# Kernel optimization log

Measured on AMD Instinct MI355X. Metric: run time of the kernel, lower is better.

## Reference

```python
import jax, jax.numpy as jnp
import numpy as np

EMBED = 512
HEADS = 8
HEAD_DIM = EMBED // HEADS
SCALE_BASE = 512
NEG = -1e9


def xpos_apply(x, offset, downscale):
    # x: [(b h), L, d]
    L, d = x.shape[1], x.shape[2]
    min_pos = -(L + offset) // 2
    max_pos = L + offset + min_pos
    base = (jnp.arange(0, d, 2, dtype=jnp.float32) + 0.4 * d) / (1.4 * d)      # [d/2]
    power = jnp.arange(min_pos, max_pos, dtype=jnp.float32) / SCALE_BASE        # [L']
    scale = base[None, :] ** power[:, None]                                     # [L', d/2]
    half = d // 2
    inv_freq = 1.0 / (10000.0 ** (jnp.arange(half, dtype=jnp.float32) / half))
    sinusoid = jnp.arange(scale.shape[0], dtype=jnp.float32)[:, None] * inv_freq[None, :]
    sin, cos = jnp.sin(sinusoid), jnp.cos(sinusoid)
    # keep last L rows (no-op when offset == 0)
    scale, sin, cos = scale[-L:], sin[-L:], cos[-L:]
    if downscale:
        scale = 1.0 / scale
    sin2 = jnp.repeat(sin * scale, 2, axis=-1)   # duplicate_interleave -> [L, d]
    cos2 = jnp.repeat(cos * scale, 2, axis=-1)
    x1, x2 = x[..., ::2], x[..., 1::2]
    rot = jnp.stack([-x2, x1], axis=-1).reshape(x.shape)  # rotate_every_two
    return x * cos2[None] + rot * sin2[None]


def split_heads(x, b, L):
    # 'b l (h d) -> (b h) l d'
    return x.reshape(b, L, HEADS, HEAD_DIM).transpose(0, 2, 1, 3).reshape(b * HEADS, L, HEAD_DIM)


def setup_inputs() -> dict:
    key = jax.random.key(0)
    ks = jax.random.split(key, 12)
    b, L = 4, 2048
    inp = {
        'query': jax.random.normal(ks[0], (b, L, EMBED), jnp.float32),
        'key': jax.random.normal(ks[1], (b, L, EMBED), jnp.float32),
        'value': jax.random.normal(ks[2], (b, L, EMBED), jnp.float32),
        'key_padding_mask': jnp.zeros((b, L), jnp.bool_),
        'attn_mask': jnp.where(jnp.tril(jnp.ones((L, L), jnp.bool_)), 0.0, NEG).astype(jnp.float32),
    }
    s = 1.0 / np.sqrt(EMBED)
    inp['Wq'] = jax.random.normal(ks[3], (EMBED, EMBED), jnp.float32) * s
    inp['bq'] = jnp.zeros((EMBED,), jnp.float32)
    inp['Wk'] = jax.random.normal(ks[4], (EMBED, EMBED), jnp.float32) * s
    inp['bk'] = jnp.zeros((EMBED,), jnp.float32)
    inp['Wv'] = jax.random.normal(ks[5], (EMBED, EMBED), jnp.float32) * s
    inp['bv'] = jnp.zeros((EMBED,), jnp.float32)
    inp['Wo'] = jax.random.normal(ks[6], (EMBED, EMBED), jnp.float32) * s
    inp['bo'] = jnp.zeros((EMBED,), jnp.float32)
    return inp


def reference(query, key, value, key_padding_mask, attn_mask, Wq, bq, Wk, bk, Wv, bv, Wo, bo):
    b, L, _ = query.shape
    q = split_heads(query @ Wq.T + bq, b, L)
    k = split_heads(key @ Wk.T + bk, b, L)
    v = split_heads(value @ Wv.T + bv, b, L)
    k = xpos_apply(k, 0, True)
    q = xpos_apply(q, 0, False)
    q = q * (HEAD_DIM ** -0.5)
    aw = jnp.einsum('btd,bsd->bts', q, k)                 # [(b h), t, s]
    aw = jnp.nan_to_num(aw) + attn_mask[None]
    aw = aw.reshape(b, HEADS, L, L)
    aw = jnp.where(key_padding_mask[:, None, None, :], jnp.finfo(aw.dtype).min, aw)
    aw = aw.reshape(b * HEADS, L, L)
    probs = jax.nn.softmax(aw.astype(jnp.float32), axis=-1).astype(aw.dtype)
    attn = jnp.einsum('bts,bsd->btd', probs, v)           # [(b h), t, d]
    attn = attn.reshape(b, HEADS, L, HEAD_DIM).transpose(0, 2, 1, 3).reshape(b, L, EMBED)
    return attn @ Wo.T + bo
```

## Files before the change

kernel.cpp:

```cpp
#include <hip/hip_runtime.h>
#include <hip/hip_bf16.h>

typedef __bf16 bf16x2 __attribute__((ext_vector_type(2)));
typedef __bf16 bf16x4 __attribute__((ext_vector_type(4)));
typedef __bf16 bf16x8 __attribute__((ext_vector_type(8)));
typedef float  f32x4  __attribute__((ext_vector_type(4)));

#define SEQ    2048
#define EMB    512
#define NHEAD  8
#define HD     64
#define NBATCH 4
#define MROWS  (NBATCH*SEQ)
#define QSCALE 0.18033688011112042f
#define INV2PI 0.15915494309189535f
#define TWOPI  6.28318530717958648f
#define NEGFREQ (-0.41524101186092028f)

__device__ __forceinline__ f32x4 mfma16(bf16x8 a, bf16x8 b, f32x4 c) {
  return __builtin_amdgcn_mfma_f32_16x16x32_bf16(a, b, c, 0, 0, 0);
}

typedef __attribute__((address_space(1))) const void gv_t;
typedef __attribute__((address_space(3))) void lv_t;
__device__ __forceinline__ void async16(const void* g, void* l) {
  __builtin_amdgcn_global_load_lds((gv_t*)g, (lv_t*)l, 16, 0, 0);
}

__global__ __launch_bounds__(256) void conv_kernel(const float* __restrict__ q,
                                                   const float* __restrict__ k,
                                                   const float* __restrict__ v,
                                                   const float* __restrict__ wq,
                                                   const float* __restrict__ wk,
                                                   const float* __restrict__ wv,
                                                   const float* __restrict__ wo,
                                                   __bf16* __restrict__ Qf,
                                                   __bf16* __restrict__ Kf,
                                                   __bf16* __restrict__ Vf,
                                                   __bf16* __restrict__ Wb,
                                                   float2* __restrict__ qtab,
                                                   float2* __restrict__ ktab) {
  const int z = blockIdx.y;
  if (z == 4) {
    if (blockIdx.x >= 256) return;
    const int t = threadIdx.x;
    const int l = blockIdx.x * 8 + (t >> 5);
    const int i = t & 31;
    const float lf = (float)l;
    const float pw = (lf - 1024.0f) * (1.0f / 512.0f);
    const float lb = __log2f((2.0f * i + 25.6f) * (1.0f / 89.6f));
    const float sc_q = __builtin_amdgcn_exp2f(pw * lb) * QSCALE;
    const float sc_k = __builtin_amdgcn_exp2f(-pw * lb);
    const float ang = lf * __builtin_amdgcn_exp2f((float)i * NEGFREQ);
    float rev = ang * INV2PI;
    rev -= floorf(rev);
    const float ar = rev * TWOPI;
    const float sn = __sinf(ar);
    const float cs = __cosf(ar);
    qtab[l * 32 + i] = float2{ cs * sc_q, sn * sc_q };
    ktab[l * 32 + i] = float2{ cs * sc_k, sn * sc_k };
    return;
  }
  const float* src;
  __bf16* dst;
  size_t i8;
  if (z < 3) {
    src = (z == 0) ? q : (z == 1) ? k : v;
    dst = (z == 0) ? Qf : (z == 1) ? Kf : Vf;
    i8 = ((size_t)blockIdx.x * 256 + threadIdx.x) * 8;
  } else {
    if (blockIdx.x >= 512) return;
    const int zw = blockIdx.x >> 7;
    src = (zw == 0) ? wq : (zw == 1) ? wk : (zw == 2) ? wv : wo;
    dst = Wb + (size_t)zw * (EMB * EMB);
    i8 = ((size_t)(blockIdx.x & 127) * 256 + threadIdx.x) * 8;
  }
  const float4 fa = ((const float4*)(src + i8))[0];
  const float4 fb = ((const float4*)(src + i8))[1];
  bf16x8 h = { (__bf16)fa.x, (__bf16)fa.y, (__bf16)fa.z, (__bf16)fa.w,
               (__bf16)fb.x, (__bf16)fb.y, (__bf16)fb.z, (__bf16)fb.w };
  *(bf16x8*)(dst + i8) = h;
}

__device__ __forceinline__ void gemm_main(const __bf16* __restrict__ A,
                                          const __bf16* __restrict__ W,
                                          __bf16* As, __bf16* Bs,
                                          f32x4 (&acc)[4][4], int m0, int n0) {
  const int tid = threadIdx.x;
  const int wid = tid >> 6, lane = tid & 63;
  const int quad = lane >> 4, l16 = lane & 15;
  const int l7 = l16 & 7;
  const int srow = lane >> 3;
  const int sxor = ((lane & 7) ^ srow) * 8;
  const int wm = (wid >> 1) * 64, wn = (wid & 1) * 64;

  #pragma unroll
  for (int i = 0; i < 4; ++i)
    #pragma unroll
    for (int j = 0; j < 4; ++j) acc[i][j] = (f32x4)(0.0f);

  for (int k0 = 0; k0 < 512; k0 += 64) {
    __syncthreads();
    #pragma unroll
    for (int ii = 0; ii < 4; ++ii) {
      const int r8 = wid * 32 + ii * 8;
      async16(A + (size_t)(m0 + r8 + srow) * 512 + k0 + sxor, &As[r8 * 64]);
      async16(W + (size_t)(n0 + r8 + srow) * 512 + k0 + sxor, &Bs[r8 * 64]);
    }
    __syncthreads();
    #pragma unroll
    for (int ks = 0; ks < 2; ++ks) {
      bf16x8 af[4], bfr[4];
      #pragma unroll
      for (int i = 0; i < 4; ++i)
        af[i] = *(const bf16x8*)&As[(wm + i * 16 + l16) * 64 +
                                    (((quad + ks * 4) ^ l7) * 8)];
      #pragma unroll
      for (int j = 0; j < 4; ++j)
        bfr[j] = *(const bf16x8*)&Bs[(wn + j * 16 + l16) * 64 +
                                     (((quad + ks * 4) ^ l7) * 8)];
      #pragma unroll
      for (int i = 0; i < 4; ++i)
        #pragma unroll
        for (int j = 0; j < 4; ++j)
          acc[i][j] = mfma16(af[i], bfr[j], acc[i][j]);
    }
  }
}

__device__ __forceinline__ void xcd_tile(int& m0, int& n0) {
  const int s = blockIdx.y * 4 + blockIdx.x;
  const int t = s >> 3;
  n0 = (t & 3) * 128;
  m0 = ((s & 7) + ((t >> 2) << 3)) * 128;
}

__global__ __launch_bounds__(256) void gemm_proj_kernel(
    const __bf16* __restrict__ Qf, const __bf16* __restrict__ Kf, const __bf16* __restrict__ Vf,
    const __bf16* __restrict__ Wb,
    const float* __restrict__ bq, const float* __restrict__ bk, const float* __restrict__ bv,
    const float2* __restrict__ qtab, const float2* __restrict__ ktab,
    __bf16* __restrict__ Qx, __bf16* __restrict__ Kx, __bf16* __restrict__ Vt) {
  __shared__ __align__(16) char smem[34816];
  __bf16* As = (__bf16*)smem;
  __bf16* Bs = (__bf16*)(smem + 16384);
  __bf16* T  = (__bf16*)smem;

  const int z = blockIdx.z;
  const __bf16* A = (z == 0) ? Qf : (z == 1) ? Kf : Vf;
  const __bf16* W = Wb + (size_t)z * (EMB * EMB);
  const float* bias = (z == 0) ? bq : (z == 1) ? bk : bv;
  int m0, n0;
  xcd_tile(m0, n0);

  f32x4 acc[4][4];
  gemm_main(A, W, As, Bs, acc, m0, n0);

  const int tid = threadIdx.x;
  const int wid = tid >> 6, lane = tid & 63;
  const int quad = lane >> 4, l16 = lane & 15;
  const int wm = (wid >> 1) * 64, wn = (wid & 1) * 64;

  __syncthreads();

  if (z == 2) {
    #pragma unroll
    for (int j = 0; j < 4; ++j) {
      const float bval = bias[n0 + wn + j * 16 + l16];
      #pragma unroll
      for (int i = 0; i < 4; ++i) {
        bf16x4 p = { (__bf16)(acc[i][j][0] + bval), (__bf16)(acc[i][j][1] + bval),
                     (__bf16)(acc[i][j][2] + bval), (__bf16)(acc[i][j][3] + bval) };
        *(bf16x4*)&T[(wn + j * 16 + l16) * 136 + wm + i * 16 + quad * 4] = p;
      }
    }
    __syncthreads();
    const int nrow = tid >> 1, mh = (tid & 1) << 6;
    bf16x8 vv[8];
    #pragma unroll
    for (int u = 0; u < 8; ++u) vv[u] = *(const bf16x8*)&T[nrow * 136 + mh + u * 8];
    const int n = n0 + nrow, h = n >> 6, d = n & 63;
    const int bb = m0 >> 11, lb2 = (m0 & 2047) + mh;
    __bf16* dst = Vt + ((size_t)(bb * 8 + h) * 64 + d) * 2048 + lb2;
    #pragma unroll
    for (int u = 0; u < 8; ++u) *(bf16x8*)(dst + u * 8) = vv[u];
  } else {
    #pragma unroll
    for (int j = 0; j < 4; ++j) {
      const float bval = bias[n0 + wn + j * 16 + l16];
      #pragma unroll
      for (int i = 0; i < 4; ++i)
        #pragma unroll
        for (int r = 0; r < 4; ++r)
          T[(wm + i * 16 + quad * 4 + r) * 136 + wn + j * 16 + l16] =
              (__bf16)(acc[i][j][r] + bval);
    }
    __syncthreads();
    const int lrow = tid >> 1, half = tid & 1;
    const int gm = m0 + lrow, l = gm & 2047, bb = gm >> 11;
    const int h = (n0 >> 6) + half;
    bf16x8 vv[8];
    #pragma unroll
    for (int u = 0; u < 8; ++u)
      vv[u] = *(const bf16x8*)&T[lrow * 136 + half * 64 + u * 8];
    bf16x8 ov[8];
    const float4* trow = (const float4*)(((z == 0) ? qtab : ktab) + l * 32);
    #pragma unroll
    for (int p = 0; p < 16; ++p) {
      const float4 cs2 = trow[p];
      const int i0 = 2 * p;
      {
        const float x1 = (float)vv[i0 >> 2][(2 * i0) & 7];
        const float x2 = (float)vv[i0 >> 2][(2 * i0 + 1) & 7];
        ov[i0 >> 2][(2 * i0) & 7]     = (__bf16)(x1 * cs2.x - x2 * cs2.y);
        ov[i0 >> 2][(2 * i0 + 1) & 7] = (__bf16)(x2 * cs2.x + x1 * cs2.y);
      }
      {
        const int i1 = i0 + 1;
        const float x1 = (float)vv[i1 >> 2][(2 * i1) & 7];
        const float x2 = (float)vv[i1 >> 2][(2 * i1 + 1) & 7];
        ov[i1 >> 2][(2 * i1) & 7]     = (__bf16)(x1 * cs2.z - x2 * cs2.w);
        ov[i1 >> 2][(2 * i1 + 1) & 7] = (__bf16)(x2 * cs2.z + x1 * cs2.w);
      }
    }
    __bf16* dst = ((z == 0) ? Qx : Kx) + ((size_t)(bb * 8 + h) * 2048 + l) * 64;
    #pragma unroll
    for (int u = 0; u < 8; ++u) *(bf16x8*)(dst + u * 8) = ov[u];
  }
}

__global__ __launch_bounds__(256) void gemm_out_kernel(
    const __bf16* __restrict__ A, const __bf16* __restrict__ W,
    const float* __restrict__ bias, float* __restrict__ C) {
  __shared__ __align__(16) char smem[34816];
  __bf16* As = (__bf16*)smem;
  __bf16* Bs = (__bf16*)(smem + 16384);
  int m0, n0;
  xcd_tile(m0, n0);
  f32x4 acc[4][4];
  gemm_main(A, W, As, Bs, acc, m0, n0);
  const int tid = threadIdx.x;
  const int wid = tid >> 6, lane = tid & 63;
  const int quad = lane >> 4, l16 = lane & 15;
  const int wm = (wid >> 1) * 64, wn = (wid & 1) * 64;
  #pragma unroll
  for (int j = 0; j < 4; ++j) {
    const int n = n0 + wn + j * 16 + l16;
    const float bval = bias[n];
    #pragma unroll
    for (int i = 0; i < 4; ++i)
      #pragma unroll
      for (int r = 0; r < 4; ++r)
        C[(size_t)(m0 + wm + i * 16 + quad * 4 + r) * 512 + n] = acc[i][j][r] + bval;
  }
}

__global__ __launch_bounds__(256) void flash_kernel(const __bf16* __restrict__ Qx,
                                                    const __bf16* __restrict__ Kx,
                                                    const __bf16* __restrict__ Vt,
                                                    const unsigned char* __restrict__ kpm,
                                                    __bf16* __restrict__ Oa) {
  __shared__ __align__(16) __bf16 Ks[2][64 * HD];
  __shared__ __align__(16) __bf16 Vs[2][64 * HD];
  __shared__ __align__(16) __bf16 Qs[64 * HD];

  const int tid = threadIdx.x;
  const int wid = tid >> 6;
  const int lane = tid & 63;
  const int quad = lane >> 4;
  const int l16 = lane & 15;
  const int l7 = l16 & 7;
  const int srow = lane >> 3;
  const int sxor = ((lane & 7) ^ srow) * 8;
  const int bh = blockIdx.x;
  const int b = bh >> 3;
  const int qb = 31 - (int)blockIdx.y;
  const int q0 = qb * 64;

  const __bf16* Qbase = Qx + (size_t)bh * (SEQ * HD);
  const __bf16* Kbase = Kx + (size_t)bh * (SEQ * HD);
  const __bf16* Vbase = Vt + (size_t)bh * (HD * SEQ);
  __bf16* Pw = Qs + wid * 1024;

  #pragma unroll
  for (int ii = 0; ii < 2; ++ii) {
    const int r0 = wid * 16 + ii * 8;
    async16(Qbase + (size_t)(q0 + r0 + srow) * HD + sxor, &Qs[r0 * HD]);
    async16(Kbase + (size_t)(r0 + srow) * HD + sxor, &Ks[0][r0 * HD]);
    async16(Vbase + (size_t)(r0 + srow) * SEQ + sxor, &Vs[0][r0 * HD]);
  }
  __syncthreads();

  const int base0 = (quad ^ l7) * 8;
  const int base1 = ((quad + 4) ^ l7) * 8;
  const int kvo0 = l16 * 64 + base0;
  const int kvo1 = l16 * 64 + base1;

  const bf16x8 qf0 = *(const bf16x8*)&Qs[(wid * 16 + l16) * HD + base0];
  const bf16x8 qf1 = *(const bf16x8*)&Qs[(wid * 16 + l16) * HD + base1];

  __bf16* const pw0 = Pw + l16 * 64 + (((0 + (quad >> 1)) ^ l7) << 3) + (quad & 1) * 4;
  __bf16* const pw1 = Pw + l16 * 64 + (((2 + (quad >> 1)) ^ l7) << 3) + (quad & 1) * 4;
  __bf16* const pw2 = Pw + l16 * 64 + (((4 + (quad >> 1)) ^ l7) << 3) + (quad & 1) * 4;
  __bf16* const pw3 = Pw + l16 * 64 + (((6 + (quad >> 1)) ^ l7) << 3) + (quad & 1) * 4;
  const __bf16* const pr0 = Pw + kvo0;
  const __bf16* const pr1 = Pw + kvo1;

  f32x4 o[4];
  #pragma unroll
  for (int i = 0; i < 4; ++i) o[i] = (f32x4)(0.0f);
  const f32x4 z4 = (f32x4)(0.0f);
  float m_run = -1e30f, l_run = 0.0f;
  const int myq = q0 + wid * 16 + l16;
  const int niter = qb + 1;

  const __bf16* kp0 = Kbase + (size_t)(64 + wid * 16 + srow) * HD + sxor;
  const __bf16* kp1 = kp0 + 8 * HD;
  const __bf16* vp0 = Vbase + (size_t)(wid * 16 + srow) * SEQ + 64 + sxor;
  const __bf16* vp1 = vp0 + 8 * SEQ;
  const unsigned char* kpmb = kpm + b * SEQ + (l16 << 2);

  int it = 0;

#define FLASH_STEP(CUR)                                                        \
  {                                                                            \
    const int kv0 = it << 6;                                                   \
    if (it + 1 < niter) {                                                      \
      async16(kp0, &Ks[1 - (CUR)][(wid * 16 + 0) * HD]);                       \
      async16(kp1, &Ks[1 - (CUR)][(wid * 16 + 8) * HD]);                       \
      async16(vp0, &Vs[1 - (CUR)][(wid * 16 + 0) * HD]);                       \
      async16(vp1, &Vs[1 - (CUR)][(wid * 16 + 8) * HD]);                       \
      kp0 += 64 * HD; kp1 += 64 * HD; vp0 += 64; vp1 += 64;                    \
    }                                                                          \
    const unsigned mine = *(const unsigned*)kpmb;                              \
    f32x4 s[4];                                                                \
    __builtin_amdgcn_s_setprio(1);                                             \
    s[0] = mfma16(*(const bf16x8*)&Ks[CUR][kvo0 +    0], qf0, z4);             \
    s[1] = mfma16(*(const bf16x8*)&Ks[CUR][kvo0 + 1024], qf0, z4);             \
    s[2] = mfma16(*(const bf16x8*)&Ks[CUR][kvo0 + 2048], qf0, z4);             \
    s[3] = mfma16(*(const bf16x8*)&Ks[CUR][kvo0 + 3072], qf0, z4);             \
    s[0] = mfma16(*(const bf16x8*)&Ks[CUR][kvo1 +    0], qf1, s[0]);           \
    s[1] = mfma16(*(const bf16x8*)&Ks[CUR][kvo1 + 1024], qf1, s[1]);           \
    s[2] = mfma16(*(const bf16x8*)&Ks[CUR][kvo1 + 2048], qf1, s[2]);           \
    s[3] = mfma16(*(const bf16x8*)&Ks[CUR][kvo1 + 3072], qf1, s[3]);           \
    __builtin_amdgcn_s_setprio(0);                                             \
                    \
    if (kv0 + 63 > q0 + wid * 16) {                                            \
      _Pragma("unroll")                                                        \
      for (int nb = 0; nb < 4; ++nb)                                           \
        _Pragma("unroll")                                                      \
        for (int r = 0; r < 4; ++r)                                            \
          if (kv0 + nb * 16 + quad * 4 + r > myq) s[nb][r] = -1e30f;           \
    }                                                                          \
                   \
    if (__any(mine != 0)) {                                                    \
      const unsigned char* kq = kpm + b * SEQ + kv0;                           \
      _Pragma("unroll")                                                        \
      for (int nb = 0; nb < 4; ++nb) {                                         \
        const unsigned pk = *(const unsigned*)(kq + nb * 16 + quad * 4);       \
        if (pk) {                                                              \
          if (pk & 0x000000FFu) s[nb][0] = -1e30f;                             \
          if (pk & 0x0000FF00u) s[nb][1] = -1e30f;                             \
          if (pk & 0x00FF0000u) s[nb][2] = -1e30f;                             \
          if (pk & 0xFF000000u) s[nb][3] = -1e30f;                             \
        }                                                                      \
      }                                                                        \
    }                                                                          \
                      \
    float mx;                                                                  \
    {                                                                          \
      f32x4 u0, u1;                                                            \
      _Pragma("unroll")                                                        \
      for (int r = 0; r < 4; ++r) u0[r] = fmaxf(s[0][r], s[1][r]);             \
      _Pragma("unroll")                                                        \
      for (int r = 0; r < 4; ++r) u1[r] = fmaxf(s[2][r], s[3][r]);             \
      _Pragma("unroll")                                                        \
      for (int r = 0; r < 4; ++r) u0[r] = fmaxf(u0[r], u1[r]);                 \
      mx = fmaxf(fmaxf(u0[0], u0[1]), fmaxf(u0[2], u0[3]));                    \
    }                                                                          \
    if (__any(mx > m_run)) {                                                   \
      float rm = fmaxf(mx, __shfl_xor(mx, 16));                                \
      rm = fmaxf(rm, __shfl_xor(rm, 32));                                      \
      const float m_new = fmaxf(m_run, rm);                                    \
      const float alpha = __builtin_amdgcn_exp2f(m_run - m_new);               \
      o[0] *= alpha; o[1] *= alpha; o[2] *= alpha; o[3] *= alpha;              \
      l_run *= alpha;                                                          \
      m_run = m_new;                                                           \
    }                                                                          \
    _Pragma("unroll")                                                          \
    for (int nb = 0; nb < 4; ++nb)                                             \
      _Pragma("unroll")                                                        \
      for (int r = 0; r < 4; ++r)                                              \
        s[nb][r] = __builtin_amdgcn_exp2f(s[nb][r] - m_run);                   \
    {                                                                          \
      f32x4 v01 = s[0] + s[1];                                                 \
      f32x4 v23 = s[2] + s[3];                                                 \
      f32x4 vt = v01 + v23;                                                    \
      l_run += (vt[0] + vt[1]) + (vt[2] + vt[3]);                              \
    }                                                                          \
           \
    *(bf16x4*)pw0 = bf16x4{ (__bf16)s[0][0], (__bf16)s[0][1],                  \
                            (__bf16)s[0][2], (__bf16)s[0][3] };                \
    *(bf16x4*)pw1 = bf16x4{ (__bf16)s[1][0], (__bf16)s[1][1],                  \
                            (__bf16)s[1][2], (__bf16)s[1][3] };                \
    *(bf16x4*)pw2 = bf16x4{ (__bf16)s[2][0], (__bf16)s[2][1],                  \
                            (__bf16)s[2][2], (__bf16)s[2][3] };                \
    *(bf16x4*)pw3 = bf16x4{ (__bf16)s[3][0], (__bf16)s[3][1],                  \
                            (__bf16)s[3][2], (__bf16)s[3][3] };                \
                                     \
    {                                                                          \
      const bf16x8 pf0 = *(const bf16x8*)pr0;                                  \
      __builtin_amdgcn_s_setprio(1);                                           \
      o[0] = mfma16(*(const bf16x8*)&Vs[CUR][kvo0 +    0], pf0, o[0]);         \
      o[1] = mfma16(*(const bf16x8*)&Vs[CUR][kvo0 + 1024], pf0, o[1]);         \
      o[2] = mfma16(*(const bf16x8*)&Vs[CUR][kvo0 + 2048], pf0, o[2]);         \
      o[3] = mfma16(*(const bf16x8*)&Vs[CUR][kvo0 + 3072], pf0, o[3]);         \
      __builtin_amdgcn_s_setprio(0);                                           \
      const bf16x8 pf1 = *(const bf16x8*)pr1;                                  \
      __builtin_amdgcn_s_setprio(1);                                           \
      o[0] = mfma16(*(const bf16x8*)&Vs[CUR][kvo1 +    0], pf1, o[0]);         \
      o[1] = mfma16(*(const bf16x8*)&Vs[CUR][kvo1 + 1024], pf1, o[1]);         \
      o[2] = mfma16(*(const bf16x8*)&Vs[CUR][kvo1 + 2048], pf1, o[2]);         \
      o[3] = mfma16(*(const bf16x8*)&Vs[CUR][kvo1 + 3072], pf1, o[3]);         \
      __builtin_amdgcn_s_setprio(0);                                           \
    }                                                                          \
    kpmb += 64;                                                                \
      \
    if (it + 1 < niter) __syncthreads();                                       \
  }

  while (it + 1 < niter) {
    FLASH_STEP(0);
    ++it;
    FLASH_STEP(1);
    ++it;
  }
  if (it < niter) {
    FLASH_STEP(0);
  }
#undef FLASH_STEP

  float lt = l_run + __shfl_xor(l_run, 16);
  lt += __shfl_xor(lt, 32);

  const float inv_l = 1.0f / lt;
  {
    bf16x4 t0 = { (__bf16)(o[0][0] * inv_l), (__bf16)(o[0][1] * inv_l),
                  (__bf16)(o[0][2] * inv_l), (__bf16)(o[0][3] * inv_l) };
    bf16x4 t1 = { (__bf16)(o[1][0] * inv_l), (__bf16)(o[1][1] * inv_l),
                  (__bf16)(o[1][2] * inv_l), (__bf16)(o[1][3] * inv_l) };
    bf16x4 t2 = { (__bf16)(o[2][0] * inv_l), (__bf16)(o[2][1] * inv_l),
                  (__bf16)(o[2][2] * inv_l), (__bf16)(o[2][3] * inv_l) };
    bf16x4 t3 = { (__bf16)(o[3][0] * inv_l), (__bf16)(o[3][1] * inv_l),
                  (__bf16)(o[3][2] * inv_l), (__bf16)(o[3][3] * inv_l) };
    *(bf16x4*)pw0 = t0;
    *(bf16x4*)pw1 = t1;
    *(bf16x4*)pw2 = t2;
    *(bf16x4*)pw3 = t3;
  }
  const int h = bh & 7;
  #pragma unroll
  for (int ii = 0; ii < 2; ++ii) {
    const int qr = ii * 8 + (lane >> 3);
    const bf16x8 ovv = *(const bf16x8*)&Pw[qr * 64 + (((lane & 7) ^ (qr & 7)) << 3)];
    *(bf16x8*)(Oa + (((size_t)b * SEQ + q0 + wid * 16 + qr) * NHEAD + h) * HD +
               (lane & 7) * 8) = ovv;
  }
}

extern "C" void kernel_launch(void* const* d_in, const int* in_sizes, int n_in,
                              void* d_out, int out_size, void* d_ws, size_t ws_size,
                              hipStream_t stream) {
  (void)in_sizes; (void)n_in; (void)out_size; (void)ws_size;
  const float* query = (const float*)d_in[0];
  const float* key   = (const float*)d_in[1];
  const float* value = (const float*)d_in[2];
  const unsigned char* kpm = (const unsigned char*)d_in[3];
  const float* Wq = (const float*)d_in[5];
  const float* bq = (const float*)d_in[6];
  const float* Wk = (const float*)d_in[7];
  const float* bk = (const float*)d_in[8];
  const float* Wv = (const float*)d_in[9];
  const float* bv = (const float*)d_in[10];
  const float* Wo = (const float*)d_in[11];
  const float* bo = (const float*)d_in[12];
  float* out = (float*)d_out;

  char* ws = (char*)d_ws;
  const size_t SZ = (size_t)MROWS * EMB * 2;
  __bf16* Qf = (__bf16*)(ws);
  __bf16* Kf = (__bf16*)(ws + SZ);
  __bf16* Vf = (__bf16*)(ws + 2 * SZ);
  __bf16* Qx = (__bf16*)(ws + 3 * SZ);
  __bf16* Kx = (__bf16*)(ws + 4 * SZ);
  __bf16* Vt = (__bf16*)(ws + 5 * SZ);
  __bf16* Wb = (__bf16*)(ws + 6 * SZ);
  float2* qtab = (float2*)(ws + 6 * SZ + 4 * (size_t)(EMB * EMB) * 2);
  float2* ktab = qtab + SEQ * 32;
  __bf16* Oa = Qf;

  conv_kernel<<<dim3(2048, 5), dim3(256), 0, stream>>>(
      query, key, value, Wq, Wk, Wv, Wo, Qf, Kf, Vf, Wb, qtab, ktab);
  gemm_proj_kernel<<<dim3(4, 64, 3), dim3(256), 0, stream>>>(
      Qf, Kf, Vf, Wb, bq, bk, bv, qtab, ktab, Qx, Kx, Vt);
  flash_kernel<<<dim3(32, 32), dim3(256), 0, stream>>>(Qx, Kx, Vt, kpm, Oa);
  gemm_out_kernel<<<dim3(4, 64), dim3(256), 0, stream>>>(
      Oa, Wb + (size_t)3 * EMB * EMB, bo, out);
}
```

Measured before the change: 207.5 us.

## Process 128-key tiles per flash iteration with single-buffered synchronous staging

The attention loop now covers 128 keys per iteration instead of 64. It reuses both halves of the K and V shared buffers as one 128-row tile, so there are fewer loop iterations and fewer barriers. The double-buffered async prefetch is replaced by staging the next tile between two barriers after compute, so global loads no longer overlap with MFMA work inside a block. The coarser causal granularity also adds some fully masked score work on diagonal tiles.

```diff
diff --git a/kernel.cpp b/kernel.cpp
--- a/kernel.cpp
+++ b/kernel.cpp
@@ -260,8 +260,8 @@
                                                     const __bf16* __restrict__ Vt,
                                                     const unsigned char* __restrict__ kpm,
                                                     __bf16* __restrict__ Oa) {
-  __shared__ __align__(16) __bf16 Ks[2][64 * HD];
-  __shared__ __align__(16) __bf16 Vs[2][64 * HD];
+  __shared__ __align__(16) __bf16 Ks[2][64 * 64];
+  __shared__ __align__(16) __bf16 Vs[2][64 * 64];
   __shared__ __align__(16) __bf16 Qs[64 * HD];
 
   const int tid = threadIdx.x;
@@ -282,13 +282,29 @@
   const __bf16* Vbase = Vt + (size_t)bh * (HD * SEQ);
   __bf16* Pw = Qs + wid * 1024;
 
+  const __bf16* kp  = Kbase + (size_t)(wid * 32 + srow) * HD + sxor;
+  const __bf16* vpA = Vbase + (size_t)(wid * 16 + srow) * SEQ + sxor;
+  const __bf16* vpB = vpA + 8 * SEQ;
+
+#define STAGE()                                                                \
+  {                                                                            \
+    async16(kp + 0 * 8 * HD, &Ks[wid >> 1][((wid & 1) * 32 +  0) * 64]);       \
+    async16(kp + 1 * 8 * HD, &Ks[wid >> 1][((wid & 1) * 32 +  8) * 64]);       \
+    async16(kp + 2 * 8 * HD, &Ks[wid >> 1][((wid & 1) * 32 + 16) * 64]);       \
+    async16(kp + 3 * 8 * HD, &Ks[wid >> 1][((wid & 1) * 32 + 24) * 64]);       \
+    async16(vpA +  0, &Vs[0][(wid * 16 + 0) * 64]);                            \
+    async16(vpA + 64, &Vs[1][(wid * 16 + 0) * 64]);                            \
+    async16(vpB +  0, &Vs[0][(wid * 16 + 8) * 64]);                            \
+    async16(vpB + 64, &Vs[1][(wid * 16 + 8) * 64]);                            \
+    kp += 128 * HD; vpA += 128; vpB += 128;                                    \
+  }
+
   #pragma unroll
   for (int ii = 0; ii < 2; ++ii) {
     const int r0 = wid * 16 + ii * 8;
     async16(Qbase + (size_t)(q0 + r0 + srow) * HD + sxor, &Qs[r0 * HD]);
-    async16(Kbase + (size_t)(r0 + srow) * HD + sxor, &Ks[0][r0 * HD]);
-    async16(Vbase + (size_t)(r0 + srow) * SEQ + sxor, &Vs[0][r0 * HD]);
-  }
+  }
+  STAGE();
   __syncthreads();
 
   const int base0 = (quad ^ l7) * 8;
@@ -312,133 +328,148 @@
   const f32x4 z4 = (f32x4)(0.0f);
   float m_run = -1e30f, l_run = 0.0f;
   const int myq = q0 + wid * 16 + l16;
-  const int niter = qb + 1;
-
-  const __bf16* kp0 = Kbase + (size_t)(64 + wid * 16 + srow) * HD + sxor;
-  const __bf16* kp1 = kp0 + 8 * HD;
-  const __bf16* vp0 = Vbase + (size_t)(wid * 16 + srow) * SEQ + 64 + sxor;
-  const __bf16* vp1 = vp0 + 8 * SEQ;
-  const unsigned char* kpmb = kpm + b * SEQ + (l16 << 2);
-
-  int it = 0;
-
-#define FLASH_STEP(CUR)                                                        \
-  {                                                                            \
-    const int kv0 = it << 6;                                                   \
-    if (it + 1 < niter) {                                                      \
-      async16(kp0, &Ks[1 - (CUR)][(wid * 16 + 0) * HD]);                       \
-      async16(kp1, &Ks[1 - (CUR)][(wid * 16 + 8) * HD]);                       \
-      async16(vp0, &Vs[1 - (CUR)][(wid * 16 + 0) * HD]);                       \
-      async16(vp1, &Vs[1 - (CUR)][(wid * 16 + 8) * HD]);                       \
-      kp0 += 64 * HD; kp1 += 64 * HD; vp0 += 64; vp1 += 64;                    \
-    }                                                                          \
-    const unsigned mine = *(const unsigned*)kpmb;                              \
-    f32x4 s[4];                                                                \
-    __builtin_amdgcn_s_setprio(1);                                             \
-    s[0] = mfma16(*(const bf16x8*)&Ks[CUR][kvo0 +    0], qf0, z4);             \
-    s[1] = mfma16(*(const bf16x8*)&Ks[CUR][kvo0 + 1024], qf0, z4);             \
-    s[2] = mfma16(*(const bf16x8*)&Ks[CUR][kvo0 + 2048], qf0, z4);             \
-    s[3] = mfma16(*(const bf16x8*)&Ks[CUR][kvo0 + 3072], qf0, z4);             \
-    s[0] = mfma16(*(const bf16x8*)&Ks[CUR][kvo1 +    0], qf1, s[0]);           \
-    s[1] = mfma16(*(const bf16x8*)&Ks[CUR][kvo1 + 1024], qf1, s[1]);           \
-    s[2] = mfma16(*(const bf16x8*)&Ks[CUR][kvo1 + 2048], qf1, s[2]);           \
-    s[3] = mfma16(*(const bf16x8*)&Ks[CUR][kvo1 + 3072], qf1, s[3]);           \
-    __builtin_amdgcn_s_setprio(0);                                             \
-                    \
-    if (kv0 + 63 > q0 + wid * 16) {                                            \
-      _Pragma("unroll")                                                        \
-      for (int nb = 0; nb < 4; ++nb)                                           \
-        _Pragma("unroll")                                                      \
-        for (int r = 0; r < 4; ++r)                                            \
-          if (kv0 + nb * 16 + quad * 4 + r > myq) s[nb][r] = -1e30f;           \
-    }                                                                          \
-                   \
-    if (__any(mine != 0)) {                                                    \
-      const unsigned char* kq = kpm + b * SEQ + kv0;                           \
-      _Pragma("unroll")                                                        \
-      for (int nb = 0; nb < 4; ++nb) {                                         \
-        const unsigned pk = *(const unsigned*)(kq + nb * 16 + quad * 4);       \
-        if (pk) {                                                              \
-          if (pk & 0x000000FFu) s[nb][0] = -1e30f;                             \
-          if (pk & 0x0000FF00u) s[nb][1] = -1e30f;                             \
-          if (pk & 0x00FF0000u) s[nb][2] = -1e30f;                             \
-          if (pk & 0xFF000000u) s[nb][3] = -1e30f;                             \
-        }                                                                      \
-      }                                                                        \
-    }                                                                          \
-                      \
-    float mx;                                                                  \
-    {                                                                          \
-      f32x4 u0, u1;                                                            \
-      _Pragma("unroll")                                                        \
-      for (int r = 0; r < 4; ++r) u0[r] = fmaxf(s[0][r], s[1][r]);             \
-      _Pragma("unroll")                                                        \
-      for (int r = 0; r < 4; ++r) u1[r] = fmaxf(s[2][r], s[3][r]);             \
-      _Pragma("unroll")                                                        \
-      for (int r = 0; r < 4; ++r) u0[r] = fmaxf(u0[r], u1[r]);                 \
-      mx = fmaxf(fmaxf(u0[0], u0[1]), fmaxf(u0[2], u0[3]));                    \
-    }                                                                          \
-    if (__any(mx > m_run)) {                                                   \
-      float rm = fmaxf(mx, __shfl_xor(mx, 16));                                \
-      rm = fmaxf(rm, __shfl_xor(rm, 32));                                      \
-      const float m_new = fmaxf(m_run, rm);                                    \
-      const float alpha = __builtin_amdgcn_exp2f(m_run - m_new);               \
-      o[0] *= alpha; o[1] *= alpha; o[2] *= alpha; o[3] *= alpha;              \
-      l_run *= alpha;                                                          \
-      m_run = m_new;                                                           \
-    }                                                                          \
-    _Pragma("unroll")                                                          \
-    for (int nb = 0; nb < 4; ++nb)                                             \
-      _Pragma("unroll")                                                        \
-      for (int r = 0; r < 4; ++r)                                              \
-        s[nb][r] = __builtin_amdgcn_exp2f(s[nb][r] - m_run);                   \
-    {                                                                          \
-      f32x4 v01 = s[0] + s[1];                                                 \
-      f32x4 v23 = s[2] + s[3];                                                 \
-      f32x4 vt = v01 + v23;                                                    \
-      l_run += (vt[0] + vt[1]) + (vt[2] + vt[3]);                              \
-    }                                                                          \
-           \
-    *(bf16x4*)pw0 = bf16x4{ (__bf16)s[0][0], (__bf16)s[0][1],                  \
-                            (__bf16)s[0][2], (__bf16)s[0][3] };                \
-    *(bf16x4*)pw1 = bf16x4{ (__bf16)s[1][0], (__bf16)s[1][1],                  \
-                            (__bf16)s[1][2], (__bf16)s[1][3] };                \
-    *(bf16x4*)pw2 = bf16x4{ (__bf16)s[2][0], (__bf16)s[2][1],                  \
-                            (__bf16)s[2][2], (__bf16)s[2][3] };                \
-    *(bf16x4*)pw3 = bf16x4{ (__bf16)s[3][0], (__bf16)s[3][1],                  \
-                            (__bf16)s[3][2], (__bf16)s[3][3] };                \
-                                     \
-    {                                                                          \
-      const bf16x8 pf0 = *(const bf16x8*)pr0;                                  \
-      __builtin_amdgcn_s_setprio(1);                                           \
-      o[0] = mfma16(*(const bf16x8*)&Vs[CUR][kvo0 +    0], pf0, o[0]);         \
-      o[1] = mfma16(*(const bf16x8*)&Vs[CUR][kvo0 + 1024], pf0, o[1]);         \
-      o[2] = mfma16(*(const bf16x8*)&Vs[CUR][kvo0 + 2048], pf0, o[2]);         \
-      o[3] = mfma16(*(const bf16x8*)&Vs[CUR][kvo0 + 3072], pf0, o[3]);         \
-      __builtin_amdgcn_s_setprio(0);                                           \
-      const bf16x8 pf1 = *(const bf16x8*)pr1;                                  \
-      __builtin_amdgcn_s_setprio(1);                                           \
-      o[0] = mfma16(*(const bf16x8*)&Vs[CUR][kvo1 +    0], pf1, o[0]);         \
-      o[1] = mfma16(*(const bf16x8*)&Vs[CUR][kvo1 + 1024], pf1, o[1]);         \
-      o[2] = mfma16(*(const bf16x8*)&Vs[CUR][kvo1 + 2048], pf1, o[2]);         \
-      o[3] = mfma16(*(const bf16x8*)&Vs[CUR][kvo1 + 3072], pf1, o[3]);         \
-      __builtin_amdgcn_s_setprio(0);                                           \
-    }                                                                          \
-    kpmb += 64;                                                                \
-      \
-    if (it + 1 < niter) __syncthreads();                                       \
-  }
-
-  while (it + 1 < niter) {
-    FLASH_STEP(0);
-    ++it;
-    FLASH_STEP(1);
-    ++it;
-  }
-  if (it < niter) {
-    FLASH_STEP(0);
-  }
-#undef FLASH_STEP
+  const int niter = (qb >> 1) + 1;
+  const unsigned char* kpmb = kpm + b * SEQ + (l16 << 3);
+
+  for (int it = 0; it < niter; ++it) {
+    const int kv0 = it << 7;
+    const uint2 mine2 = *(const uint2*)kpmb;
+
+    f32x4 s[8];
+    __builtin_amdgcn_s_setprio(1);
+    s[0] = mfma16(*(const bf16x8*)&Ks[0][kvo0 +    0], qf0, z4);
+    s[1] = mfma16(*(const bf16x8*)&Ks[0][kvo0 + 1024], qf0, z4);
+    s[2] = mfma16(*(const bf16x8*)&Ks[0][kvo0 + 2048], qf0, z4);
+    s[3] = mfma16(*(const bf16x8*)&Ks[0][kvo0 + 3072], qf0, z4);
+    s[4] = mfma16(*(const bf16x8*)&Ks[1][kvo0 +    0], qf0, z4);
+    s[5] = mfma16(*(const bf16x8*)&Ks[1][kvo0 + 1024], qf0, z4);
+    s[6] = mfma16(*(const bf16x8*)&Ks[1][kvo0 + 2048], qf0, z4);
+    s[7] = mfma16(*(const bf16x8*)&Ks[1][kvo0 + 3072], qf0, z4);
+    s[0] = mfma16(*(const bf16x8*)&Ks[0][kvo1 +    0], qf1, s[0]);
+    s[1] = mfma16(*(const bf16x8*)&Ks[0][kvo1 + 1024], qf1, s[1]);
+    s[2] = mfma16(*(const bf16x8*)&Ks[0][kvo1 + 2048], qf1, s[2]);
+    s[3] = mfma16(*(const bf16x8*)&Ks[0][kvo1 + 3072], qf1, s[3]);
+    s[4] = mfma16(*(const bf16x8*)&Ks[1][kvo1 +    0], qf1, s[4]);
+    s[5] = mfma16(*(const bf16x8*)&Ks[1][kvo1 + 1024], qf1, s[5]);
+    s[6] = mfma16(*(const bf16x8*)&Ks[1][kvo1 + 2048], qf1, s[6]);
+    s[7] = mfma16(*(const bf16x8*)&Ks[1][kvo1 + 3072], qf1, s[7]);
+    __builtin_amdgcn_s_setprio(0);
+
+    if (kv0 + 127 > q0 + wid * 16) {
+      #pragma unroll
+      for (int nb = 0; nb < 8; ++nb)
+        #pragma unroll
+        for (int r = 0; r < 4; ++r)
+          if (kv0 + nb * 16 + quad * 4 + r > myq) s[nb][r] = -1e30f;
+    }
+    if (__any((mine2.x | mine2.y) != 0)) {
+      const unsigned char* kq = kpm + b * SEQ + kv0;
+      #pragma unroll
+      for (int nb = 0; nb < 8; ++nb) {
+        const unsigned pk = *(const unsigned*)(kq + nb * 16 + quad * 4);
+        if (pk) {
+          if (pk & 0x000000FFu) s[nb][0] = -1e30f;
+          if (pk & 0x0000FF00u) s[nb][1] = -1e30f;
+          if (pk & 0x00FF0000u) s[nb][2] = -1e30f;
+          if (pk & 0xFF000000u) s[nb][3] = -1e30f;
+        }
+      }
+    }
+
+    float mx;
+    {
+      f32x4 u0, u1, u2, u3;
+      #pragma unroll
+      for (int r = 0; r < 4; ++r) u0[r] = fmaxf(s[0][r], s[1][r]);
+      #pragma unroll
+      for (int r = 0; r < 4; ++r) u1[r] = fmaxf(s[2][r], s[3][r]);
+      #pragma unroll
+      for (int r = 0; r < 4; ++r) u2[r] = fmaxf(s[4][r], s[5][r]);
+      #pragma unroll
+      for (int r = 0; r < 4; ++r) u3[r] = fmaxf(s[6][r], s[7][r]);
+      #pragma unroll
+      for (int r = 0; r < 4; ++r) u0[r] = fmaxf(fmaxf(u0[r], u1[r]),
+                                                fmaxf(u2[r], u3[r]));
+      mx = fmaxf(fmaxf(u0[0], u0[1]), fmaxf(u0[2], u0[3]));
+    }
+    if (__any(mx > m_run)) {
+      float rm = fmaxf(mx, __shfl_xor(mx, 16));
+      rm = fmaxf(rm, __shfl_xor(rm, 32));
+      const float m_new = fmaxf(m_run, rm);
+      const float alpha = __builtin_amdgcn_exp2f(m_run - m_new);
+      o[0] *= alpha; o[1] *= alpha; o[2] *= alpha; o[3] *= alpha;
+      l_run *= alpha;
+      m_run = m_new;
+    }
+    #pragma unroll
+    for (int nb = 0; nb < 8; ++nb)
+      #pragma unroll
+      for (int r = 0; r < 4; ++r)
+        s[nb][r] = __builtin_amdgcn_exp2f(s[nb][r] - m_run);
+    {
+      f32x4 va = (s[0] + s[1]) + (s[2] + s[3]);
+      f32x4 vb = (s[4] + s[5]) + (s[6] + s[7]);
+      f32x4 vt = va + vb;
+      l_run += (vt[0] + vt[1]) + (vt[2] + vt[3]);
+    }
+
+    *(bf16x4*)pw0 = bf16x4{ (__bf16)s[0][0], (__bf16)s[0][1],
+                            (__bf16)s[0][2], (__bf16)s[0][3] };
+    *(bf16x4*)pw1 = bf16x4{ (__bf16)s[1][0], (__bf16)s[1][1],
+                            (__bf16)s[1][2], (__bf16)s[1][3] };
+    *(bf16x4*)pw2 = bf16x4{ (__bf16)s[2][0], (__bf16)s[2][1],
+                            (__bf16)s[2][2], (__bf16)s[2][3] };
+    *(bf16x4*)pw3 = bf16x4{ (__bf16)s[3][0], (__bf16)s[3][1],
+                            (__bf16)s[3][2], (__bf16)s[3][3] };
+    {
+      const bf16x8 pf0 = *(const bf16x8*)pr0;
+      __builtin_amdgcn_s_setprio(1);
+      o[0] = mfma16(*(const bf16x8*)&Vs[0][kvo0 +    0], pf0, o[0]);
+      o[1] = mfma16(*(const bf16x8*)&Vs[0][kvo0 + 1024], pf0, o[1]);
+      o[2] = mfma16(*(const bf16x8*)&Vs[0][kvo0 + 2048], pf0, o[2]);
+      o[3] = mfma16(*(const bf16x8*)&Vs[0][kvo0 + 3072], pf0, o[3]);
+      __builtin_amdgcn_s_setprio(0);
+      const bf16x8 pf1 = *(const bf16x8*)pr1;
+      __builtin_amdgcn_s_setprio(1);
+      o[0] = mfma16(*(const bf16x8*)&Vs[0][kvo1 +    0], pf1, o[0]);
+      o[1] = mfma16(*(const bf16x8*)&Vs[0][kvo1 + 1024], pf1, o[1]);
+      o[2] = mfma16(*(const bf16x8*)&Vs[0][kvo1 + 2048], pf1, o[2]);
+      o[3] = mfma16(*(const bf16x8*)&Vs[0][kvo1 + 3072], pf1, o[3]);
+      __builtin_amdgcn_s_setprio(0);
+    }
+    *(bf16x4*)pw0 = bf16x4{ (__bf16)s[4][0], (__bf16)s[4][1],
+                            (__bf16)s[4][2], (__bf16)s[4][3] };
+    *(bf16x4*)pw1 = bf16x4{ (__bf16)s[5][0], (__bf16)s[5][1],
+                            (__bf16)s[5][2], (__bf16)s[5][3] };
+    *(bf16x4*)pw2 = bf16x4{ (__bf16)s[6][0], (__bf16)s[6][1],
+                            (__bf16)s[6][2], (__bf16)s[6][3] };
+    *(bf16x4*)pw3 = bf16x4{ (__bf16)s[7][0], (__bf16)s[7][1],
+                            (__bf16)s[7][2], (__bf16)s[7][3] };
+    {
+      const bf16x8 pf0 = *(const bf16x8*)pr0;
+      __builtin_amdgcn_s_setprio(1);
+      o[0] = mfma16(*(const bf16x8*)&Vs[1][kvo0 +    0], pf0, o[0]);
+      o[1] = mfma16(*(const bf16x8*)&Vs[1][kvo0 + 1024], pf0, o[1]);
+      o[2] = mfma16(*(const bf16x8*)&Vs[1][kvo0 + 2048], pf0, o[2]);
+      o[3] = mfma16(*(const bf16x8*)&Vs[1][kvo0 + 3072], pf0, o[3]);
+      __builtin_amdgcn_s_setprio(0);
+      const bf16x8 pf1 = *(const bf16x8*)pr1;
+      __builtin_amdgcn_s_setprio(1);
+      o[0] = mfma16(*(const bf16x8*)&Vs[1][kvo1 +    0], pf1, o[0]);
+      o[1] = mfma16(*(const bf16x8*)&Vs[1][kvo1 + 1024], pf1, o[1]);
+      o[2] = mfma16(*(const bf16x8*)&Vs[1][kvo1 + 2048], pf1, o[2]);
+      o[3] = mfma16(*(const bf16x8*)&Vs[1][kvo1 + 3072], pf1, o[3]);
+      __builtin_amdgcn_s_setprio(0);
+    }
+    kpmb += 128;
+
+    if (it + 1 < niter) {
+      __syncthreads();
+      STAGE();
+      __syncthreads();
+    }
+  }
+#undef STAGE
 
   float lt = l_run + __shfl_xor(l_run, 16);
   lt += __shfl_xor(lt, 32);
```

New measurement: 199.3 us. -3.9%, faster.
